# Kernel optimization log

Measured on AMD Instinct MI355X. Metric: run time of the kernel, lower is better.

The kernel has to match this reference:

```python
import jax, jax.numpy as jnp
import numpy as np

N_NODES = 30000
N_EDGES = 150000
N_REL = 10
IN_DIM = 256
OUT_DIM = 256


def setup_inputs() -> dict:
    key = jax.random.key(0)
    ks = jax.random.split(key, 10)
    s = 1.0 / np.sqrt(IN_DIM)  # ~nn.Linear init scale
    return {
        "x": jax.random.normal(ks[0], (N_NODES, IN_DIM), jnp.float32),
        "W_self": jax.random.uniform(ks[1], (IN_DIM, OUT_DIM), jnp.float32, -s, s),
        "b_self": jax.random.uniform(ks[2], (OUT_DIM,), jnp.float32, -s, s),
        "W_fwd": jax.random.uniform(ks[3], (N_REL, IN_DIM, OUT_DIM), jnp.float32, -s, s),
        "b_fwd": jax.random.uniform(ks[4], (N_REL, OUT_DIM), jnp.float32, -s, s),
        "W_rev": jax.random.uniform(ks[5], (N_REL, IN_DIM, OUT_DIM), jnp.float32, -s, s),
        "b_rev": jax.random.uniform(ks[6], (N_REL, OUT_DIM), jnp.float32, -s, s),
        "dep_idx": jax.random.randint(ks[7], (N_EDGES,), 0, N_NODES, jnp.int32),
        "rel_idx": jax.random.randint(ks[8], (N_EDGES,), 0, N_REL, jnp.int32),
        "gov_idx": jax.random.randint(ks[9], (N_EDGES,), 0, N_NODES, jnp.int32),
    }


def reference(x, W_self, b_self, W_fwd, b_fwd, W_rev, b_rev, dep_idx, rel_idx, gov_idx):
    # self transform for every token: [N, out]
    out = x @ W_self + b_self
    # transform all nodes by every relation weight up-front: [R, N, out]
    H_fwd = jnp.einsum("ni,rio->rno", x, W_fwd) + b_fwd[:, None, :]
    H_rev = jnp.einsum("ni,rio->rno", x, W_rev) + b_rev[:, None, :]
    # per-edge gather: forward msg uses governor feature, reverse msg uses dependent
    msg_fwd = H_fwd[rel_idx, gov_idx]  # [E, out]
    msg_rev = H_rev[rel_idx, dep_idx]  # [E, out]
    # scatter-add: forward msg -> dependent, reverse msg -> governor
    out = out.at[dep_idx].add(msg_fwd)
    out = out.at[gov_idx].add(msg_rev)
    return out
```

## Files before the change

kernel.cpp:

```cpp
#include <hip/hip_runtime.h>

#define N_NODES 30000
#define N_EDGES 150000
#define N_REL 10
#define DIM 256

#define SORT_BLOCKS 120
#define SORT_CHUNK ((N_EDGES + SORT_BLOCKS - 1) / SORT_BLOCKS)

#define SCAN_CHUNK 256
#define SCAN_BLOCKS ((N_NODES + SCAN_CHUNK - 1) / SCAN_CHUNK)

#define A_STRIDE 280

#define PREP_XB 7500
#define PREP_WB 5376
#define PREP_ZB 235

typedef __attribute__((ext_vector_type(8))) short bf16x8;
typedef __attribute__((ext_vector_type(4))) float f32x4;

__device__ __forceinline__ unsigned short f2bf(float f) {
  union { float f; unsigned int u; } v; v.f = f;
  unsigned int u = v.u;
  unsigned int r = u + 0x7fffu + ((u >> 16) & 1u);
  return (unsigned short)(r >> 16);
}


__global__ void prep_kernel(const float* __restrict__ x,
                            const float* __restrict__ Wf,
                            const float* __restrict__ Wr,
                            const float* __restrict__ Ws,
                            unsigned short* __restrict__ xbf,
                            unsigned short* __restrict__ wt,
                            int* __restrict__ cnt) {
  int b = blockIdx.x;
  if (b < PREP_XB) {
    int idx = b * 256 + threadIdx.x;
    float4 v = reinterpret_cast<const float4*>(x)[idx];
    ushort4 o;
    o.x = f2bf(v.x); o.y = f2bf(v.y); o.z = f2bf(v.z); o.w = f2bf(v.w);
    reinterpret_cast<ushort4*>(xbf)[idx] = o;
  } else if (b < PREP_XB + PREP_WB) {
    int idx = (b - PREP_XB) * 256 + threadIdx.x;
    int bb = idx >> 16;
    int t = idx & 65535;
    int o = t >> 8, i = t & 255;
    const float* src = (bb < N_REL) ? (Wf + (size_t)bb * 65536)
                     : (bb < 2 * N_REL) ? (Wr + (size_t)(bb - N_REL) * 65536)
                     : Ws;
    wt[idx] = f2bf(src[i * 256 + o]);
  } else {
    int i = (b - PREP_XB - PREP_WB) * 256 + threadIdx.x;
    if (i < 2 * N_NODES) cnt[i] = 0;
  }
}

__global__ void hist_all_kernel(const int* __restrict__ rel,
                                const int* __restrict__ dep,
                                const int* __restrict__ gov,
                                int* __restrict__ block_counts,
                                int* __restrict__ cnt) {
  __shared__ int h[N_REL];
  if (threadIdx.x < N_REL) h[threadIdx.x] = 0;
  __syncthreads();
  int beg = blockIdx.x * SORT_CHUNK;
  int end = min(beg + SORT_CHUNK, N_EDGES);
  for (int e = beg + threadIdx.x; e < end; e += blockDim.x) {
    atomicAdd(&h[rel[e]], 1);
    atomicAdd(&cnt[dep[e]], 1);
    atomicAdd(&cnt[N_NODES + gov[e]], 1);
  }
  __syncthreads();
  if (threadIdx.x < N_REL)
    block_counts[blockIdx.x * N_REL + threadIdx.x] = h[threadIdx.x];
}

__global__ void scan_rel_kernel(const int* __restrict__ block_counts,
                                int* __restrict__ rel_start,
                                int* __restrict__ block_offset) {
  __shared__ int tot[N_REL];
  int r = threadIdx.x;
  if (r < N_REL) {
    int s = 0;
    for (int b = 0; b < SORT_BLOCKS; ++b) s += block_counts[b * N_REL + r];
    tot[r] = s;
  }
  __syncthreads();
  if (threadIdx.x == 0) {
    int s = 0;
    for (int i = 0; i < N_REL; ++i) { rel_start[i] = s; s += tot[i]; }
    rel_start[N_REL] = s;
  }
  __syncthreads();
  if (r < N_REL) {
    int run = rel_start[r];
    for (int b = 0; b < SORT_BLOCKS; ++b) {
      block_offset[b * N_REL + r] = run;
      run += block_counts[b * N_REL + r];
    }
  }
}

__global__ void scanA_kernel(const int* __restrict__ cnt,
                             int* __restrict__ tmp, int* __restrict__ sums) {
  __shared__ int s[SCAN_CHUNK];
  int d = blockIdx.y, b = blockIdx.x, t = threadIdx.x;
  int i = b * SCAN_CHUNK + t;
  int v = (i < N_NODES) ? cnt[d * N_NODES + i] : 0;
  s[t] = v;
  __syncthreads();
  for (int off = 1; off < SCAN_CHUNK; off <<= 1) {
    int add = (t >= off) ? s[t - off] : 0;
    __syncthreads();
    s[t] += add;
    __syncthreads();
  }
  if (i < N_NODES) tmp[d * N_NODES + i] = s[t] - v;
  if (t == SCAN_CHUNK - 1) sums[d * SCAN_BLOCKS + b] = s[t];
}

__global__ void scanB_kernel(const int* __restrict__ sums,
                             int* __restrict__ chunk_off, int* __restrict__ rp) {
  __shared__ int s[128];
  int d = blockIdx.x, t = threadIdx.x;
  int v = (t < SCAN_BLOCKS) ? sums[d * SCAN_BLOCKS + t] : 0;
  s[t] = v;
  __syncthreads();
  for (int off = 1; off < 128; off <<= 1) {
    int add = (t >= off) ? s[t - off] : 0;
    __syncthreads();
    s[t] += add;
    __syncthreads();
  }
  if (t < SCAN_BLOCKS) chunk_off[d * SCAN_BLOCKS + t] = s[t] - v;
  if (t == 127) rp[d * (N_NODES + 1) + N_NODES] = s[127];
}

__global__ void scanC_kernel(const int* __restrict__ tmp,
                             const int* __restrict__ chunk_off,
                             int* __restrict__ rp, int* __restrict__ cursor) {
  int d = blockIdx.y;
  int i = blockIdx.x * SCAN_CHUNK + threadIdx.x;
  if (i < N_NODES) {
    int v = tmp[d * N_NODES + i] + chunk_off[d * SCAN_BLOCKS + blockIdx.x];
    rp[d * (N_NODES + 1) + i] = v;
    cursor[d * N_NODES + i] = v;
  }
}

__global__ void scatter_all_kernel(const int* __restrict__ rel,
                                   const int* __restrict__ dep,
                                   const int* __restrict__ gov,
                                   const int* __restrict__ block_offset,
                                   int* __restrict__ cursor,
                                   int* __restrict__ perm,
                                   int* __restrict__ colf,
                                   int* __restrict__ colr) {
  __shared__ int cur[N_REL];
  if (threadIdx.x < N_REL)
    cur[threadIdx.x] = block_offset[blockIdx.x * N_REL + threadIdx.x];
  __syncthreads();
  int beg = blockIdx.x * SORT_CHUNK;
  int end = min(beg + SORT_CHUNK, N_EDGES);
  for (int e = beg + threadIdx.x; e < end; e += blockDim.x) {
    int pos = atomicAdd(&cur[rel[e]], 1);
    perm[pos] = e;
    colf[atomicAdd(&cursor[dep[e]], 1)] = pos;
    colr[atomicAdd(&cursor[N_NODES + gov[e]], 1)] = pos;
  }
}


__global__ __launch_bounds__(256, 2)
void mega_gemm_kernel(const unsigned short* __restrict__ xbf,
                      const unsigned short* __restrict__ wt,
                      const float* __restrict__ b_self,
                      const float* __restrict__ b_fwd,
                      const float* __restrict__ b_rev,
                      const int* __restrict__ perm,
                      const int* __restrict__ rel_start,
                      const int* __restrict__ dep,
                      const int* __restrict__ gov,
                      unsigned short* __restrict__ msg,
                      float* __restrict__ out) {
  const int bkt = blockIdx.y;
  const bool is_self = (bkt == 2 * N_REL);
  const int r = bkt % N_REL;
  const bool fwd = bkt < N_REL;

  int beg, cnt;
  const int* src_idx = fwd ? gov : dep;
  unsigned short* mdir = msg + (fwd ? 0 : (size_t)N_EDGES * DIM);
  if (is_self) { beg = 0; cnt = N_NODES; }
  else { beg = rel_start[r]; cnt = rel_start[r + 1] - beg; }
  const int ntiles = (cnt + 63) >> 6;

  const int tid = threadIdx.x;
  const int wave = tid >> 6, lane = tid & 63;
  const int lm = lane & 15, q = lane >> 4;
  const int nb = wave * 64;

  __shared__ int s_src[64];
  __shared__ unsigned short sA[64 * A_STRIDE];

  bf16x8 wf[8][4];
  const unsigned short* wbase = wt + (size_t)bkt * DIM * DIM;
  #pragma unroll
  for (int kk = 0; kk < 8; ++kk)
    #pragma unroll
    for (int ni = 0; ni < 4; ++ni)
      wf[kk][ni] = *reinterpret_cast<const bf16x8*>(
          wbase + (size_t)(nb + ni * 16 + lm) * DIM + kk * 32 + q * 8);

  const float* bptr = is_self ? b_self : ((fwd ? b_fwd : b_rev) + r * DIM);
  float bias[4];
  #pragma unroll
  for (int ni = 0; ni < 4; ++ni) bias[ni] = bptr[nb + ni * 16 + lm];

  for (int t = blockIdx.x; t < ntiles; t += gridDim.x) {
    const int tile0 = t << 6;
    const int rows_valid = min(64, cnt - tile0);

    if (tid < 64) {
      int s;
      if (is_self) {
        int rr = tile0 + tid;
        s = rr < N_NODES ? rr : N_NODES - 1;
      } else {
        s = (tid < rows_valid) ? src_idx[perm[beg + tile0 + tid]] : 0;
      }
      s_src[tid] = s;
    }
    __syncthreads();

    {
      int half = lane >> 5;
      int lcol = lane & 31;
      #pragma unroll
      for (int i = 0; i < 8; ++i) {
        int row = wave * 16 + i * 2 + half;
        uint4 v = *reinterpret_cast<const uint4*>(
            xbf + (size_t)s_src[row] * DIM + lcol * 8);
        *reinterpret_cast<uint4*>(sA + row * A_STRIDE + lcol * 8) = v;
      }
    }
    __syncthreads();

    f32x4 acc[4][4];
    #pragma unroll
    for (int mi = 0; mi < 4; ++mi)
      #pragma unroll
      for (int ni = 0; ni < 4; ++ni)
        acc[mi][ni] = (f32x4){0.f, 0.f, 0.f, 0.f};

    #pragma unroll
    for (int kk = 0; kk < 8; ++kk) {
      bf16x8 a[4];
      #pragma unroll
      for (int mi = 0; mi < 4; ++mi)
        a[mi] = *reinterpret_cast<const bf16x8*>(
            sA + (mi * 16 + lm) * A_STRIDE + kk * 32 + q * 8);
      #pragma unroll
      for (int mi = 0; mi < 4; ++mi)
        #pragma unroll
        for (int ni = 0; ni < 4; ++ni)
          acc[mi][ni] = __builtin_amdgcn_mfma_f32_16x16x32_bf16(a[mi], wf[kk][ni], acc[mi][ni], 0, 0, 0);
    }

    if (is_self) {
      #pragma unroll
      for (int mi = 0; mi < 4; ++mi) {
        #pragma unroll
        for (int reg = 0; reg < 4; ++reg) {
          int row = mi * 16 + q * 4 + reg;
          if (row < rows_valid) {
            #pragma unroll
            for (int ni = 0; ni < 4; ++ni)
              out[(size_t)(tile0 + row) * DIM + nb + ni * 16 + lm] =
                  acc[mi][ni][reg] + bias[ni];
          }
        }
      }
    } else {
      #pragma unroll
      for (int mi = 0; mi < 4; ++mi) {
        #pragma unroll
        for (int reg = 0; reg < 4; ++reg) {
          int row = mi * 16 + q * 4 + reg;
          if (row < rows_valid) {
            unsigned int p0 = ((unsigned int)f2bf(acc[mi][1][reg] + bias[1]) << 16) |
                              f2bf(acc[mi][0][reg] + bias[0]);
            unsigned int p1 = ((unsigned int)f2bf(acc[mi][3][reg] + bias[3]) << 16) |
                              f2bf(acc[mi][2][reg] + bias[2]);
            uint2 u; u.x = p0; u.y = p1;
            *reinterpret_cast<uint2*>(
                mdir + (size_t)(beg + tile0 + row) * DIM + nb + lm * 4) = u;
          }
        }
      }
    }
    __syncthreads();
  }
}


__global__ void reduce_both_kernel(const unsigned short* __restrict__ msg,
                                   const int* __restrict__ rp,
                                   const int* __restrict__ colf,
                                   const int* __restrict__ colr,
                                   float* __restrict__ out) {
  const int n = blockIdx.x, t = threadIdx.x;
  const int g = t >> 6, lane = t & 63;
  const int b0 = rp[n], e0 = rp[n + 1];
  const int b1 = rp[(N_NODES + 1) + n], e1 = rp[(N_NODES + 1) + n + 1];
  if (e0 <= b0 && e1 <= b1) return;

  float a0 = 0.f, a1 = 0.f, a2 = 0.f, a3 = 0.f;
  for (int j = b0 + g; j < e0; j += 4) {
    int row = colf[j];
    uint2 v = *reinterpret_cast<const uint2*>(msg + (size_t)row * DIM + lane * 4);
    union { unsigned int u; float f; } c;
    c.u = v.x << 16;          a0 += c.f;
    c.u = v.x & 0xffff0000u;  a1 += c.f;
    c.u = v.y << 16;          a2 += c.f;
    c.u = v.y & 0xffff0000u;  a3 += c.f;
  }
  for (int j = b1 + g; j < e1; j += 4) {
    int row = colr[j];
    uint2 v = *reinterpret_cast<const uint2*>(
        msg + (size_t)(N_EDGES + row) * DIM + lane * 4);
    union { unsigned int u; float f; } c;
    c.u = v.x << 16;          a0 += c.f;
    c.u = v.x & 0xffff0000u;  a1 += c.f;
    c.u = v.y << 16;          a2 += c.f;
    c.u = v.y & 0xffff0000u;  a3 += c.f;
  }

  __shared__ float part[4][DIM];
  const int cb = (lane >> 4) * 64 + (lane & 15);
  part[g][cb +  0] = a0;
  part[g][cb + 16] = a1;
  part[g][cb + 32] = a2;
  part[g][cb + 48] = a3;
  __syncthreads();
  float s = part[0][t] + part[1][t] + part[2][t] + part[3][t];
  out[(size_t)n * DIM + t] += s;
}


__global__ __launch_bounds__(256, 2)
void self_gemm_kernel(const unsigned short* __restrict__ xbf,
                      const unsigned short* __restrict__ wt_self,
                      const float* __restrict__ b_self,
                      float* __restrict__ out) {
  const int tid = threadIdx.x;
  const int wave = tid >> 6, lane = tid & 63;
  const int lm = lane & 15, q = lane >> 4;
  const int nb = wave * 64;

  bf16x8 wf[8][4];
  #pragma unroll
  for (int kk = 0; kk < 8; ++kk)
    #pragma unroll
    for (int ni = 0; ni < 4; ++ni)
      wf[kk][ni] = *reinterpret_cast<const bf16x8*>(
          wt_self + (size_t)(nb + ni * 16 + lm) * DIM + kk * 32 + q * 8);

  float bias[4];
  #pragma unroll
  for (int ni = 0; ni < 4; ++ni) bias[ni] = b_self[nb + ni * 16 + lm];

  const int ntiles = (N_NODES + 63) / 64;
  for (int t = blockIdx.x; t < ntiles; t += gridDim.x) {
    const int row0 = t * 64;
    const unsigned short* xr[4];
    #pragma unroll
    for (int mi = 0; mi < 4; ++mi) {
      int r = row0 + mi * 16 + lm;
      int rc = r < N_NODES ? r : N_NODES - 1;
      xr[mi] = xbf + (size_t)rc * DIM + q * 8;
    }

    f32x4 acc[4][4];
    #pragma unroll
    for (int mi = 0; mi < 4; ++mi)
      #pragma unroll
      for (int ni = 0; ni < 4; ++ni)
        acc[mi][ni] = (f32x4){0.f, 0.f, 0.f, 0.f};

    #pragma unroll
    for (int kk = 0; kk < 8; ++kk) {
      bf16x8 a[4];
      #pragma unroll
      for (int mi = 0; mi < 4; ++mi)
        a[mi] = *reinterpret_cast<const bf16x8*>(xr[mi] + kk * 32);
      #pragma unroll
      for (int mi = 0; mi < 4; ++mi)
        #pragma unroll
        for (int ni = 0; ni < 4; ++ni)
          acc[mi][ni] = __builtin_amdgcn_mfma_f32_16x16x32_bf16(a[mi], wf[kk][ni], acc[mi][ni], 0, 0, 0);
    }

    #pragma unroll
    for (int mi = 0; mi < 4; ++mi) {
      #pragma unroll
      for (int reg = 0; reg < 4; ++reg) {
        int row = row0 + mi * 16 + q * 4 + reg;
        if (row < N_NODES) {
          #pragma unroll
          for (int ni = 0; ni < 4; ++ni)
            out[(size_t)row * DIM + nb + ni * 16 + lm] = acc[mi][ni][reg] + bias[ni];
        }
      }
    }
  }
}

__global__ void edge_gemm_atomic_kernel(const unsigned short* __restrict__ xbf,
                                        const unsigned short* __restrict__ wt,
                                        const float* __restrict__ b_fwd,
                                        const float* __restrict__ b_rev,
                                        const int* __restrict__ perm,
                                        const int* __restrict__ rel_start,
                                        const int* __restrict__ dep,
                                        const int* __restrict__ gov,
                                        float* __restrict__ out) {
  const int bucket = blockIdx.y;
  const int r = bucket % N_REL;
  const bool fwd = bucket < N_REL;
  const int beg = rel_start[r];
  const int cnt = rel_start[r + 1] - beg;
  const int ntiles = (cnt + 63) >> 6;

  const int tid = threadIdx.x;
  const int wave = tid >> 6, lane = tid & 63;
  const int lm = lane & 15, q = lane >> 4;
  const int nb = wave * 64;

  __shared__ int s_src[64], s_dst[64];

  const unsigned short* wr[4];
  #pragma unroll
  for (int ni = 0; ni < 4; ++ni)
    wr[ni] = wt + (size_t)bucket * DIM * DIM + (size_t)(nb + ni * 16 + lm) * DIM + q * 8;

  const float* bptr = (fwd ? b_fwd : b_rev) + r * DIM;
  float bias[4];
  #pragma unroll
  for (int ni = 0; ni < 4; ++ni) bias[ni] = bptr[nb + ni * 16 + lm];

  for (int t = blockIdx.x; t < ntiles; t += gridDim.x) {
    const int tile0 = t << 6;
    const int rows_valid = min(64, cnt - tile0);

    if (tid < 64) {
      int s = 0, d = -1;
      if (tid < rows_valid) {
        int e = perm[beg + tile0 + tid];
        int gv = gov[e], dp = dep[e];
        s = fwd ? gv : dp;
        d = fwd ? dp : gv;
      }
      s_src[tid] = s;
      s_dst[tid] = d;
    }
    __syncthreads();

    const unsigned short* xr[4];
    #pragma unroll
    for (int mi = 0; mi < 4; ++mi)
      xr[mi] = xbf + (size_t)s_src[mi * 16 + lm] * DIM + q * 8;

    f32x4 acc[4][4];
    #pragma unroll
    for (int mi = 0; mi < 4; ++mi)
      #pragma unroll
      for (int ni = 0; ni < 4; ++ni)
        acc[mi][ni] = (f32x4){0.f, 0.f, 0.f, 0.f};

    #pragma unroll
    for (int k0 = 0; k0 < DIM; k0 += 32) {
      bf16x8 a[4], b[4];
      #pragma unroll
      for (int mi = 0; mi < 4; ++mi) a[mi] = *reinterpret_cast<const bf16x8*>(xr[mi] + k0);
      #pragma unroll
      for (int ni = 0; ni < 4; ++ni) b[ni] = *reinterpret_cast<const bf16x8*>(wr[ni] + k0);
      #pragma unroll
      for (int mi = 0; mi < 4; ++mi)
        #pragma unroll
        for (int ni = 0; ni < 4; ++ni)
          acc[mi][ni] = __builtin_amdgcn_mfma_f32_16x16x32_bf16(a[mi], b[ni], acc[mi][ni], 0, 0, 0);
    }

    #pragma unroll
    for (int mi = 0; mi < 4; ++mi) {
      #pragma unroll
      for (int reg = 0; reg < 4; ++reg) {
        int row = mi * 16 + q * 4 + reg;
        if (row < rows_valid) {
          int dst = s_dst[row];
          float* op = out + (size_t)dst * DIM + nb + lm;
          #pragma unroll
          for (int ni = 0; ni < 4; ++ni)
            atomicAdd(op + ni * 16, acc[mi][ni][reg] + bias[ni]);
        }
      }
    }
    __syncthreads();
  }
}


extern "C" void kernel_launch(void* const* d_in, const int* in_sizes, int n_in,
                              void* d_out, int out_size, void* d_ws, size_t ws_size,
                              hipStream_t stream) {
  const float* x      = (const float*)d_in[0];
  const float* W_self = (const float*)d_in[1];
  const float* b_self = (const float*)d_in[2];
  const float* W_fwd  = (const float*)d_in[3];
  const float* b_fwd  = (const float*)d_in[4];
  const float* W_rev  = (const float*)d_in[5];
  const float* b_rev  = (const float*)d_in[6];
  const int* dep = (const int*)d_in[7];
  const int* rel = (const int*)d_in[8];
  const int* gov = (const int*)d_in[9];
  float* out = (float*)d_out;

  char* base = (char*)d_ws;
  size_t off = 0;
  auto alloc = [&](size_t bytes) -> char* {
    char* p = base + off;
    off = (off + bytes + 15) & ~(size_t)15;
    return p;
  };

  unsigned short* xbf = (unsigned short*)alloc((size_t)N_NODES * DIM * 2);
  unsigned short* wt  = (unsigned short*)alloc((size_t)21 * DIM * DIM * 2);
  int* perm          = (int*)alloc((size_t)N_EDGES * 4);
  int* rel_start     = (int*)alloc(16 * 4);
  int* block_counts  = (int*)alloc(SORT_BLOCKS * N_REL * 4);
  int* block_offset  = (int*)alloc(SORT_BLOCKS * N_REL * 4);
  int* cnt       = (int*)alloc((size_t)2 * N_NODES * 4);
  int* tmp       = (int*)alloc((size_t)2 * N_NODES * 4);
  int* sums      = (int*)alloc((size_t)2 * SCAN_BLOCKS * 4);
  int* chunk_off = (int*)alloc((size_t)2 * SCAN_BLOCKS * 4);
  int* rp        = (int*)alloc((size_t)2 * (N_NODES + 1) * 4);
  int* cursor    = (int*)alloc((size_t)2 * N_NODES * 4);
  int* colf      = (int*)alloc((size_t)N_EDGES * 4);
  int* colr      = (int*)alloc((size_t)N_EDGES * 4);
  unsigned short* msg = (unsigned short*)alloc((size_t)2 * N_EDGES * DIM * 2);
  const bool two_phase = (off <= ws_size);

  prep_kernel<<<PREP_XB + PREP_WB + PREP_ZB, 256, 0, stream>>>(
      x, W_fwd, W_rev, W_self, xbf, wt, cnt);
  hist_all_kernel<<<SORT_BLOCKS, 256, 0, stream>>>(rel, dep, gov, block_counts, cnt);
  scan_rel_kernel<<<1, 64, 0, stream>>>(block_counts, rel_start, block_offset);
  scanA_kernel<<<dim3(SCAN_BLOCKS, 2), SCAN_CHUNK, 0, stream>>>(cnt, tmp, sums);
  scanB_kernel<<<2, 128, 0, stream>>>(sums, chunk_off, rp);
  scanC_kernel<<<dim3(SCAN_BLOCKS, 2), SCAN_CHUNK, 0, stream>>>(tmp, chunk_off, rp, cursor);
  scatter_all_kernel<<<SORT_BLOCKS, 256, 0, stream>>>(
      rel, dep, gov, block_offset, cursor, perm, colf, colr);

  if (two_phase) {
    mega_gemm_kernel<<<dim3(48, 2 * N_REL + 1), 256, 0, stream>>>(
        xbf, wt, b_self, b_fwd, b_rev, perm, rel_start, dep, gov, msg, out);
    reduce_both_kernel<<<N_NODES, 256, 0, stream>>>(msg, rp, colf, colr, out);
  } else {
    self_gemm_kernel<<<120, 256, 0, stream>>>(
        xbf, wt + (size_t)20 * DIM * DIM, b_self, out);
    edge_gemm_atomic_kernel<<<dim3(260, 20), 256, 0, stream>>>(
        xbf, wt, b_fwd, b_rev, perm, rel_start, dep, gov, out);
  }
}
```

Before: 284.8 us.

## Prefetch next gather tile in registers, precompute source indices, split self GEMM

The scatter kernel now writes per-position source node indices (srcf/srcr), so the GEMM no longer needs the double indirection through perm and dep/gov. The GEMM loop is software-pipelined: the next tile's row indices and gathered x rows are loaded into registers while the current tile's MFMAs run, and the trailing barrier is dropped. The self-transform bucket is split into two halves so its work spreads over more blocks. The cost is more registers for the prefetch buffers, which may hurt occupancy at the launch bound of 2, plus two extra index arrays written during scatter.

```diff
diff --git a/kernel.cpp b/kernel.cpp
--- a/kernel.cpp
+++ b/kernel.cpp
@@ -156,6 +156,8 @@
                                    const int* __restrict__ block_offset,
                                    int* __restrict__ cursor,
                                    int* __restrict__ perm,
+                                   int* __restrict__ srcf,
+                                   int* __restrict__ srcr,
                                    int* __restrict__ colf,
                                    int* __restrict__ colr) {
   __shared__ int cur[N_REL];
@@ -165,10 +167,13 @@
   int beg = blockIdx.x * SORT_CHUNK;
   int end = min(beg + SORT_CHUNK, N_EDGES);
   for (int e = beg + threadIdx.x; e < end; e += blockDim.x) {
+    int dp = dep[e], gv = gov[e];
     int pos = atomicAdd(&cur[rel[e]], 1);
     perm[pos] = e;
-    colf[atomicAdd(&cursor[dep[e]], 1)] = pos;
-    colr[atomicAdd(&cursor[N_NODES + gov[e]], 1)] = pos;
+    srcf[pos] = gv;
+    srcr[pos] = dp;
+    colf[atomicAdd(&cursor[dp], 1)] = pos;
+    colr[atomicAdd(&cursor[N_NODES + gv], 1)] = pos;
   }
 }
 
@@ -179,34 +184,41 @@
                       const float* __restrict__ b_self,
                       const float* __restrict__ b_fwd,
                       const float* __restrict__ b_rev,
-                      const int* __restrict__ perm,
+                      const int* __restrict__ srcf,
+                      const int* __restrict__ srcr,
                       const int* __restrict__ rel_start,
-                      const int* __restrict__ dep,
-                      const int* __restrict__ gov,
                       unsigned short* __restrict__ msg,
                       float* __restrict__ out) {
   const int bkt = blockIdx.y;
-  const bool is_self = (bkt == 2 * N_REL);
-  const int r = bkt % N_REL;
+  const bool is_self = (bkt >= 2 * N_REL);
   const bool fwd = bkt < N_REL;
+  const int r = is_self ? 0 : (fwd ? bkt : bkt - N_REL);
 
   int beg, cnt;
-  const int* src_idx = fwd ? gov : dep;
+  const int* src_arr = fwd ? srcf : srcr;
   unsigned short* mdir = msg + (fwd ? 0 : (size_t)N_EDGES * DIM);
-  if (is_self) { beg = 0; cnt = N_NODES; }
-  else { beg = rel_start[r]; cnt = rel_start[r + 1] - beg; }
+  if (is_self) {
+    beg = (bkt - 2 * N_REL) * (N_NODES / 2);
+    cnt = N_NODES / 2;
+  } else {
+    beg = rel_start[r];
+    cnt = rel_start[r + 1] - beg;
+  }
   const int ntiles = (cnt + 63) >> 6;
+  const int GX = gridDim.x;
 
   const int tid = threadIdx.x;
   const int wave = tid >> 6, lane = tid & 63;
   const int lm = lane & 15, q = lane >> 4;
   const int nb = wave * 64;
+  const int half = lane >> 5;
+  const int lcol = lane & 31;
 
   __shared__ int s_src[64];
   __shared__ unsigned short sA[64 * A_STRIDE];
 
   bf16x8 wf[8][4];
-  const unsigned short* wbase = wt + (size_t)bkt * DIM * DIM;
+  const unsigned short* wbase = wt + (size_t)(is_self ? 2 * N_REL : bkt) * DIM * DIM;
   #pragma unroll
   for (int kk = 0; kk < 8; ++kk)
     #pragma unroll
@@ -219,34 +231,55 @@
   #pragma unroll
   for (int ni = 0; ni < 4; ++ni) bias[ni] = bptr[nb + ni * 16 + lm];
 
-  for (int t = blockIdx.x; t < ntiles; t += gridDim.x) {
+  int t = blockIdx.x;
+  if (t >= ntiles) return;
+
+  auto load_idx = [&](int tt) -> int {
+    int tile0_ = tt << 6;
+    if (is_self) {
+      int rr = beg + tile0_ + tid;
+      return rr < beg + cnt ? rr : beg + cnt - 1;
+    } else {
+      int p_ = tile0_ + tid;
+      p_ = p_ < cnt ? p_ : cnt - 1;
+      return src_arr[beg + p_];
+    }
+  };
+  auto issue_D = [&](uint4* d) {
+    #pragma unroll
+    for (int i = 0; i < 8; ++i) {
+      int row = wave * 16 + i * 2 + half;
+      d[i] = *reinterpret_cast<const uint4*>(
+          xbf + (size_t)s_src[row] * DIM + lcol * 8);
+    }
+  };
+  auto write_A = [&](const uint4* d) {
+    #pragma unroll
+    for (int i = 0; i < 8; ++i) {
+      int row = wave * 16 + i * 2 + half;
+      *reinterpret_cast<uint4*>(sA + row * A_STRIDE + lcol * 8) = d[i];
+    }
+  };
+
+  int idxreg = 0;
+  if (tid < 64) s_src[tid] = load_idx(t);
+  __syncthreads();
+  uint4 d[8];
+  issue_D(d);
+  if (tid < 64 && t + GX < ntiles) idxreg = load_idx(t + GX);
+
+  for (; t < ntiles; t += GX) {
     const int tile0 = t << 6;
     const int rows_valid = min(64, cnt - tile0);
-
-    if (tid < 64) {
-      int s;
-      if (is_self) {
-        int rr = tile0 + tid;
-        s = rr < N_NODES ? rr : N_NODES - 1;
-      } else {
-        s = (tid < rows_valid) ? src_idx[perm[beg + tile0 + tid]] : 0;
-      }
-      s_src[tid] = s;
-    }
-    __syncthreads();
-
-    {
-      int half = lane >> 5;
-      int lcol = lane & 31;
-      #pragma unroll
-      for (int i = 0; i < 8; ++i) {
-        int row = wave * 16 + i * 2 + half;
-        uint4 v = *reinterpret_cast<const uint4*>(
-            xbf + (size_t)s_src[row] * DIM + lcol * 8);
-        *reinterpret_cast<uint4*>(sA + row * A_STRIDE + lcol * 8) = v;
-      }
-    }
-    __syncthreads();
+    const bool have_next = (t + GX) < ntiles;
+    const bool have_next2 = (t + 2 * GX) < ntiles;
+
+    __syncthreads();
+    if (tid < 64 && have_next) s_src[tid] = idxreg;
+    write_A(d);
+    if (tid < 64 && have_next2) idxreg = load_idx(t + 2 * GX);
+    __syncthreads();
+    if (have_next) issue_D(d);
 
     f32x4 acc[4][4];
     #pragma unroll
@@ -278,7 +311,7 @@
           if (row < rows_valid) {
             #pragma unroll
             for (int ni = 0; ni < 4; ++ni)
-              out[(size_t)(tile0 + row) * DIM + nb + ni * 16 + lm] =
+              out[(size_t)(beg + tile0 + row) * DIM + nb + ni * 16 + lm] =
                   acc[mi][ni][reg] + bias[ni];
           }
         }
@@ -301,7 +334,6 @@
         }
       }
     }
-    __syncthreads();
   }
 }
 
@@ -539,6 +571,8 @@
   unsigned short* xbf = (unsigned short*)alloc((size_t)N_NODES * DIM * 2);
   unsigned short* wt  = (unsigned short*)alloc((size_t)21 * DIM * DIM * 2);
   int* perm          = (int*)alloc((size_t)N_EDGES * 4);
+  int* srcf          = (int*)alloc((size_t)N_EDGES * 4);
+  int* srcr          = (int*)alloc((size_t)N_EDGES * 4);
   int* rel_start     = (int*)alloc(16 * 4);
   int* block_counts  = (int*)alloc(SORT_BLOCKS * N_REL * 4);
   int* block_offset  = (int*)alloc(SORT_BLOCKS * N_REL * 4);
@@ -561,11 +595,11 @@
   scanB_kernel<<<2, 128, 0, stream>>>(sums, chunk_off, rp);
   scanC_kernel<<<dim3(SCAN_BLOCKS, 2), SCAN_CHUNK, 0, stream>>>(tmp, chunk_off, rp, cursor);
   scatter_all_kernel<<<SORT_BLOCKS, 256, 0, stream>>>(
-      rel, dep, gov, block_offset, cursor, perm, colf, colr);
+      rel, dep, gov, block_offset, cursor, perm, srcf, srcr, colf, colr);
 
   if (two_phase) {
-    mega_gemm_kernel<<<dim3(48, 2 * N_REL + 1), 256, 0, stream>>>(
-        xbf, wt, b_self, b_fwd, b_rev, perm, rel_start, dep, gov, msg, out);
+    mega_gemm_kernel<<<dim3(48, 2 * N_REL + 2), 256, 0, stream>>>(
+        xbf, wt, b_self, b_fwd, b_rev, srcf, srcr, rel_start, msg, out);
     reduce_both_kernel<<<N_NODES, 256, 0, stream>>>(msg, rp, colf, colr, out);
   } else {
     self_gemm_kernel<<<120, 256, 0, stream>>>(
```

After: 323.7 us. +13.6%, slower.
